# Kernel tuning notes

Measured on AMD Instinct MI355X. Metric: run time of the kernel, lower is better.

The kernel has to match this reference:

```python
import jax, jax.numpy as jnp
import numpy as np

B = 16384   # batch
D = 768     # in_features == out_features
H = 768     # expert_hidden_size (must equal D, see MoRALayer wiring)
E = 4       # num_experts_per_level
L = 2       # num_levels
K = 2       # SparseMoE top-k
T = 10      # max_act_steps
LN_EPS = 1e-5


def setup_inputs() -> dict:
    key = jax.random.key(0)
    ks = jax.random.split(key, 8)
    s = 0.02
    return {
        "x": jax.random.normal(ks[0], (B, D), jnp.float32),
        # LSTMCell params (torch gate order i,f,g,o)
        "Wi": jax.random.normal(ks[1], (4 * H, D), jnp.float32) * s,
        "Wh": jax.random.normal(ks[2], (4 * H, H), jnp.float32) * s,
        "bi": jnp.zeros((4 * H,), jnp.float32),
        "bh": jnp.zeros((4 * H,), jnp.float32),
        # halting head
        "Whalt": jax.random.normal(ks[3], (1, H), jnp.float32) * s,
        "bhalt": jnp.zeros((1,), jnp.float32),
        # hierarchical MoE params, stacked over levels (all dims equal: D==H)
        "gateW": jax.random.normal(ks[4], (L, E, H), jnp.float32) * s,
        "gateb": jnp.zeros((L, E), jnp.float32),
        "W1": jax.random.normal(ks[5], (L, E, H, H), jnp.float32) * s,
        "b1": jnp.zeros((L, E, H), jnp.float32),
        "W2": jax.random.normal(ks[6], (L, E, D, H), jnp.float32) * s,
        "b2": jnp.zeros((L, E, D), jnp.float32),
        # LayerNorm
        "gamma": jnp.ones((D,), jnp.float32),
        "beta": jnp.zeros((D,), jnp.float32),
    }


def _act(x, Wi, Wh, bi, bh, Whalt, bhalt):
    """AdaptiveComputationTime: fixed T LSTM steps (faithful worst-case of the
    data-dependent early break). Returns rem * mean_t(h_t) per the torch math:
    avg = sum_t(h_t * rem_final) / n_updates, with rem_final broadcast over t."""
    b = x.shape[0]
    h0 = jnp.zeros((b, H), x.dtype)
    c0 = jnp.zeros((b, H), x.dtype)
    hp0 = jnp.zeros((b, 1), x.dtype)
    rem0 = jnp.zeros((b, 1), x.dtype)
    hsum0 = jnp.zeros((b, H), x.dtype)
    xWi = x @ Wi.T + bi + bh  # constant across steps

    def step(carry, _):
        h, c, hp, rem, hsum = carry
        gates = xWi + h @ Wh.T
        i, f, g, o = jnp.split(gates, 4, axis=-1)
        c = jax.nn.sigmoid(f) * c + jax.nn.sigmoid(i) * jnp.tanh(g)
        h = jax.nn.sigmoid(o) * jnp.tanh(c)
        y = jax.nn.sigmoid(h @ Whalt.T + bhalt)  # [b,1]
        hp = hp + y * (1.0 - hp)
        rem = rem + 1.0 - hp
        return (h, c, hp, rem, hsum + h), None

    (h, c, hp, rem, hsum), _ = jax.lax.scan(
        step, (h0, c0, hp0, rem0, hsum0), None, length=T)
    n_updates = jnp.asarray(float(T), x.dtype)
    avg = rem * hsum / n_updates  # [b,H]
    return avg, hp, n_updates


def _sparse_moe(x, Wg, bg, W1, b1, W2, b2):
    """Top-k expert routing (intended semantics of the torch SparseMoE)."""
    logits = x @ Wg.T + bg                                   # [b,E]
    w, idx = jax.lax.top_k(logits, K)                        # [b,K]
    w = jax.nn.softmax(w, axis=-1)
    hmid = jax.nn.relu(jnp.einsum('bi,ehi->beh', x, W1) + b1)  # [b,E,H]
    eo = jnp.einsum('beh,eoh->beo', hmid, W2) + b2             # [b,E,D]
    sel = jnp.take_along_axis(eo, idx[:, :, None], axis=1)     # [b,K,D]
    return jnp.sum(w[:, :, None] * sel, axis=1)                # [b,D]


def reference(x, Wi, Wh, bi, bh, Whalt, bhalt,
              gateW, gateb, W1, b1, W2, b2, gamma, beta):
    h, _hp, _n = _act(x, Wi, Wh, bi, bh, Whalt, bhalt)
    for l in range(L):
        h = _sparse_moe(h, gateW[l], gateb[l], W1[l], b1[l], W2[l], b2[l])
    mu = jnp.mean(h, axis=-1, keepdims=True)
    var = jnp.mean(jnp.square(h - mu), axis=-1, keepdims=True)
    return (h - mu) * jax.lax.rsqrt(var + LN_EPS) * gamma + beta
```

## Files before the change

### kernel.cpp

```cpp
#include <hip/hip_runtime.h>
#include <cstdint>
#include <cstddef>

#define Bn 16384
#define Dn 768
#define Hn 768
#define G4 3072
#define Tn 10
#define LO_SCALE 4096.0f
#define LO_INV   (1.0f/4096.0f)

typedef _Float16 f16;
typedef _Float16 f16x8 __attribute__((ext_vector_type(8)));
typedef float    f32x4 __attribute__((ext_vector_type(4)));

__device__ __forceinline__ float fexp2(float x) { return __builtin_amdgcn_exp2f(x); }
__device__ __forceinline__ float frcp(float x)  { return __builtin_amdgcn_rcpf(x); }
__device__ __forceinline__ float fsigm(float x) { return frcp(1.f + fexp2(-1.44269504f * x)); }
__device__ __forceinline__ float ftanh(float x) { return 1.f - 2.f * frcp(1.f + fexp2(2.88539008f * x)); }

__device__ __forceinline__ void gll16(const void* g, void* l) {
    __builtin_amdgcn_global_load_lds((const __attribute__((address_space(1))) void*)g,
                                     (__attribute__((address_space(3))) void*)l, 16, 0, 0);
}

template <bool SPLIT, int EPI, bool BIAS, bool RELU>
__global__ __launch_bounds__(256) void mgemm(
    const f16* __restrict__ Ah, const f16* __restrict__ Al, int lda,
    const f16* __restrict__ Bh, const f16* __restrict__ Bl,
    float* __restrict__ Cf, f16* __restrict__ Ch, f16* __restrict__ Cl, int ldc,
    const float* __restrict__ bias,
    const float* __restrict__ xwi, float* __restrict__ cst, float* __restrict__ hsum,
    f16* __restrict__ hh_out, f16* __restrict__ hl_out,
    float* __restrict__ dhalt, const float* __restrict__ Whalt,
    long aZ, long bZ, long cZ, long biasZ)
{
    const int z = blockIdx.z;
    if (z) {
        Ah += (long)z * aZ; if (SPLIT) Al += (long)z * aZ;
        Bh += (long)z * bZ; if (SPLIT) Bl += (long)z * bZ;
        if (EPI == 0) Cf += (long)z * cZ;
        if (EPI == 1 || EPI == 2) { Ch += (long)z * cZ; if (EPI == 1) Cl += (long)z * cZ; }
        if (BIAS) bias += (long)z * biasZ;
    }
    constexpr int HALF = SPLIT ? 2 : 1;
    __shared__ __align__(16) f16 sA[2][HALF * 4096];
    __shared__ __align__(16) f16 sB[2][HALF * 4096];

    const int tid  = threadIdx.x;
    const int w    = tid >> 6, lane = tid & 63;
    const int quad = lane >> 4, l15 = lane & 15;
    const int n0 = blockIdx.x * 128, m0 = blockIdx.y * 128;
    const int wm = (w >> 1) * 64,   wn = (w & 1) * 64;

    const int sr0 = tid >> 2;
    const int sc0 = (((tid & 3) - (sr0 >> 1)) & 3);
    const int sr1 = (tid + 256) >> 2;
    const int sc1 = (((tid & 3) - (sr1 >> 1)) & 3);

    auto stage = [&](int sel, int k0) {
        gll16(Ah + (long)(m0 + sr0) * lda + k0 + sc0 * 8, &sA[sel][tid * 8]);
        gll16(Bh + (long)(n0 + sr0) * 768 + k0 + sc0 * 8, &sB[sel][tid * 8]);
        gll16(Ah + (long)(m0 + sr1) * lda + k0 + sc1 * 8, &sA[sel][(tid + 256) * 8]);
        gll16(Bh + (long)(n0 + sr1) * 768 + k0 + sc1 * 8, &sB[sel][(tid + 256) * 8]);
        if (SPLIT) {
            gll16(Al + (long)(m0 + sr0) * lda + k0 + sc0 * 8, &sA[sel][4096 + tid * 8]);
            gll16(Bl + (long)(n0 + sr0) * 768 + k0 + sc0 * 8, &sB[sel][4096 + tid * 8]);
            gll16(Al + (long)(m0 + sr1) * lda + k0 + sc1 * 8, &sA[sel][4096 + (tid + 256) * 8]);
            gll16(Bl + (long)(n0 + sr1) * 768 + k0 + sc1 * 8, &sB[sel][4096 + (tid + 256) * 8]);
        }
    };

    f32x4 acc[4][4], accx[4][4];
#pragma unroll
    for (int i = 0; i < 4; i++)
#pragma unroll
        for (int j = 0; j < 4; j++) {
            acc[i][j] = (f32x4){0.f, 0.f, 0.f, 0.f};
            if (SPLIT) accx[i][j] = (f32x4){0.f, 0.f, 0.f, 0.f};
        }

    stage(0, 0);
    for (int it = 0; it < 24; it++) {
        __syncthreads();
        if (it + 1 < 24) stage((it + 1) & 1, (it + 1) * 32);
        const int sel = it & 1;

        f16x8 ah[4], al[4], bh[4], bl[4];
#pragma unroll
        for (int t = 0; t < 4; t++) {
            int ra = wm + t * 16 + l15;
            int ca = (quad + (ra >> 1)) & 3;
            ah[t] = *(const f16x8*)&sA[sel][ra * 32 + ca * 8];
            if (SPLIT) al[t] = *(const f16x8*)&sA[sel][4096 + ra * 32 + ca * 8];
            int rb = wn + t * 16 + l15;
            int cb = (quad + (rb >> 1)) & 3;
            bh[t] = *(const f16x8*)&sB[sel][rb * 32 + cb * 8];
            if (SPLIT) bl[t] = *(const f16x8*)&sB[sel][4096 + rb * 32 + cb * 8];
        }
#pragma unroll
        for (int i = 0; i < 4; i++)
#pragma unroll
            for (int j = 0; j < 4; j++) {
                acc[i][j] = __builtin_amdgcn_mfma_f32_16x16x32_f16(ah[i], bh[j], acc[i][j], 0, 0, 0);
                if (SPLIT) {
                    accx[i][j] = __builtin_amdgcn_mfma_f32_16x16x32_f16(ah[i], bl[j], accx[i][j], 0, 0, 0);
                    accx[i][j] = __builtin_amdgcn_mfma_f32_16x16x32_f16(al[i], bh[j], accx[i][j], 0, 0, 0);
                }
            }
    }

    if (EPI == 3) {
        const int j = ((n0 + wn) >> 2) + l15;
        const float wj = Whalt[j];
#pragma unroll
        for (int i = 0; i < 4; i++) {
#pragma unroll
            for (int reg = 0; reg < 4; reg++) {
                int r = m0 + wm + i * 16 + quad * 4 + reg;
                long xb = (long)r * G4 + n0 + wn + l15;
                float iv = acc[i][0][reg] + accx[i][0][reg] * LO_INV + xwi[xb];
                float fv = acc[i][1][reg] + accx[i][1][reg] * LO_INV + xwi[xb + 16];
                float gv = acc[i][2][reg] + accx[i][2][reg] * LO_INV + xwi[xb + 32];
                float ov = acc[i][3][reg] + accx[i][3][reg] * LO_INV + xwi[xb + 48];
                long ci = (long)r * Hn + j;
                float cv = fsigm(fv) * cst[ci] + fsigm(iv) * ftanh(gv);
                float hv = fsigm(ov) * ftanh(cv);
                cst[ci] = cv;
                hsum[ci] += hv;
                f16 hh = (f16)hv;
                hh_out[ci] = hh;
                hl_out[ci] = (f16)((hv - (float)hh) * LO_SCALE);
                float p = hv * wj;
                p += __shfl_xor(p, 1, 16);
                p += __shfl_xor(p, 2, 16);
                p += __shfl_xor(p, 4, 16);
                p += __shfl_xor(p, 8, 16);
                if (l15 == 0) atomicAdd(&dhalt[r], p);
            }
        }
    } else {
#pragma unroll
        for (int i = 0; i < 4; i++)
#pragma unroll
            for (int j = 0; j < 4; j++) {
                int col = n0 + wn + j * 16 + l15;
                float bv = BIAS ? bias[col] : 0.f;
#pragma unroll
                for (int reg = 0; reg < 4; reg++) {
                    int r = m0 + wm + i * 16 + quad * 4 + reg;
                    float v = acc[i][j][reg] + (SPLIT ? accx[i][j][reg] * LO_INV : 0.f) + bv;
                    if (RELU) v = v > 0.f ? v : 0.f;
                    long o = (long)r * ldc + col;
                    if (EPI == 0) Cf[o] = v;
                    else if (EPI == 2) Ch[o] = (f16)v;
                    else {
                        f16 hh = (f16)v;
                        Ch[o] = hh;
                        Cl[o] = (f16)((v - (float)hh) * LO_SCALE);
                    }
                }
            }
    }
}


__global__ void split_plain_k(const float* __restrict__ src, f16* __restrict__ dh,
                              f16* __restrict__ dl, long n) {
    long i = (long)blockIdx.x * 256 + threadIdx.x;
    if (i < n) {
        float v = src[i];
        f16 h = (f16)v;
        dh[i] = h;
        dl[i] = (f16)((v - (float)h) * LO_SCALE);
    }
}

__global__ void split_perm_k(const float* __restrict__ src, f16* __restrict__ dh,
                             f16* __restrict__ dl) {
    int P = blockIdx.x;
    int q = ((P >> 4) & 3) * Hn + (P >> 6) * 16 + (P & 15);
    const float* s = src + (long)q * 768;
    long o = (long)P * 768;
#pragma unroll
    for (int u = 0; u < 3; u++) {
        int kk = threadIdx.x + u * 256;
        float v = s[kk];
        f16 h = (f16)v;
        dh[o + kk] = h;
        dl[o + kk] = (f16)((v - (float)h) * LO_SCALE);
    }
}

__global__ void bsum_perm_k(const float* __restrict__ bi, const float* __restrict__ bh,
                            float* __restrict__ bsum) {
    int P = blockIdx.x * 256 + threadIdx.x;
    if (P < G4) {
        int q = ((P >> 4) & 3) * Hn + (P >> 6) * 16 + (P & 15);
        bsum[P] = bi[q] + bh[q];
    }
}

__global__ __launch_bounds__(256) void lstm0_k(
    const float* __restrict__ xwi, float* __restrict__ cst, float* __restrict__ hsum,
    f16* __restrict__ hh, f16* __restrict__ hl, float* __restrict__ d0,
    const float* __restrict__ Whalt)
{
    const int row = blockIdx.x, tid = threadIdx.x;
    const float* xr = xwi + (long)row * G4;
    const long hb = (long)row * Hn;
    float part = 0.f;
#pragma unroll
    for (int u = 0; u < 3; u++) {
        int j = tid + u * 256;
        int Pb = (j >> 4) * 64 + (j & 15);
        float iv = xr[Pb], gv = xr[Pb + 32], ov = xr[Pb + 48];
        float cv = fsigm(iv) * ftanh(gv);
        float hv = fsigm(ov) * ftanh(cv);
        cst[hb + j] = cv;
        hsum[hb + j] = hv;
        f16 h = (f16)hv;
        hh[hb + j] = h;
        hl[hb + j] = (f16)((hv - (float)h) * LO_SCALE);
        part += hv * Whalt[j];
    }
    __shared__ float red[256];
    red[tid] = part;
    __syncthreads();
    for (int s = 128; s > 0; s >>= 1) {
        if (tid < s) red[tid] += red[tid + s];
        __syncthreads();
    }
    if (tid == 0) d0[row] = red[0];
}

__global__ void rem_k(const float* __restrict__ d, const float* __restrict__ bhalt,
                      float* __restrict__ rem, int bc) {
    int r = blockIdx.x * 256 + threadIdx.x;
    if (r >= bc) return;
    float b0 = bhalt[0];
    float prod = 1.f, rm = 0.f;
#pragma unroll
    for (int t = 0; t < Tn; t++) {
        float y = fsigm(d[(long)t * bc + r] + b0);
        prod *= (1.f - y);
        rm += prod;
    }
    rem[r] = rm;
}

__global__ void avgsplit_k(const float* __restrict__ hsum, const float* __restrict__ rem,
                           f16* __restrict__ xmh, f16* __restrict__ xml) {
    long i = (long)blockIdx.x * 256 + threadIdx.x;
    int row = (int)(i / Hn);
    float v = rem[row] * hsum[i] * (1.f / (float)Tn);
    f16 h = (f16)v;
    xmh[i] = h;
    xml[i] = (f16)((v - (float)h) * LO_SCALE);
}

__global__ __launch_bounds__(256) void moe_gate_k(
    const f16* __restrict__ xmh, const f16* __restrict__ xml,
    const float* __restrict__ gW, const float* __restrict__ gb,
    float* __restrict__ wout, int* __restrict__ idxout)
{
    const int row = blockIdx.x, tid = threadIdx.x;
    const long xb = (long)row * Hn;
    float p[4] = {0.f, 0.f, 0.f, 0.f};
#pragma unroll
    for (int u = 0; u < 3; u++) {
        int j = tid + u * 256;
        float xv = (float)xmh[xb + j] + (float)xml[xb + j] * LO_INV;
        p[0] += xv * gW[j];
        p[1] += xv * gW[Hn + j];
        p[2] += xv * gW[2 * Hn + j];
        p[3] += xv * gW[3 * Hn + j];
    }
    __shared__ float red[256];
    __shared__ float logit[4];
    for (int e = 0; e < 4; e++) {
        red[tid] = p[e];
        __syncthreads();
        for (int s = 128; s > 0; s >>= 1) {
            if (tid < s) red[tid] += red[tid + s];
            __syncthreads();
        }
        if (tid == 0) logit[e] = red[0] + gb[e];
        __syncthreads();
    }
    if (tid == 0) {
        int i0 = 0;
        for (int e = 1; e < 4; e++) if (logit[e] > logit[i0]) i0 = e;
        int i1 = -1;
        for (int e = 0; e < 4; e++) {
            if (e == i0) continue;
            if (i1 < 0 || logit[e] > logit[i1]) i1 = e;
        }
        float ex = expf(logit[i1] - logit[i0]);
        wout[2 * row] = 1.f / (1.f + ex);
        wout[2 * row + 1] = ex / (1.f + ex);
        idxout[2 * row] = i0;
        idxout[2 * row + 1] = i1;
    }
}

template <bool SO>
__global__ void combine_k(const float* __restrict__ eo, const float* __restrict__ wv,
                          const int* __restrict__ idx, float* __restrict__ dst,
                          f16* __restrict__ dh, f16* __restrict__ dl) {
    long i = (long)blockIdx.x * 256 + threadIdx.x;
    int row = (int)(i / Hn);
    int d = (int)(i - (long)row * Hn);
    long base = (long)row * G4;
    float v = wv[2 * row]     * eo[base + (long)idx[2 * row]     * Hn + d]
            + wv[2 * row + 1] * eo[base + (long)idx[2 * row + 1] * Hn + d];
    if (SO) {
        f16 h = (f16)v;
        dh[i] = h;
        dl[i] = (f16)((v - (float)h) * LO_SCALE);
    } else {
        dst[i] = v;
    }
}

__global__ __launch_bounds__(256) void layernorm_k(
    const float* __restrict__ in, const float* __restrict__ gamma,
    const float* __restrict__ beta, float* __restrict__ out)
{
    const int row = blockIdx.x, tid = threadIdx.x;
    const float* xr = in + (long)row * Dn;
    float v[3], s = 0.f, s2 = 0.f;
#pragma unroll
    for (int u = 0; u < 3; u++) {
        v[u] = xr[tid + u * 256];
        s += v[u];
        s2 += v[u] * v[u];
    }
    __shared__ float r1[256], r2[256];
    __shared__ float smu, srs;
    r1[tid] = s; r2[tid] = s2;
    __syncthreads();
    for (int st = 128; st > 0; st >>= 1) {
        if (tid < st) { r1[tid] += r1[tid + st]; r2[tid] += r2[tid + st]; }
        __syncthreads();
    }
    if (tid == 0) {
        float mu = r1[0] * (1.f / (float)Dn);
        float var = r2[0] * (1.f / (float)Dn) - mu * mu;
        smu = mu;
        srs = 1.f / sqrtf(var + 1e-5f);
    }
    __syncthreads();
    float mu = smu, rs = srs;
#pragma unroll
    for (int u = 0; u < 3; u++) {
        int j = tid + u * 256;
        out[(long)row * Dn + j] = (v[u] - mu) * rs * gamma[j] + beta[j];
    }
}


extern "C" void kernel_launch(void* const* d_in, const int* in_sizes, int n_in,
                              void* d_out, int out_size, void* d_ws, size_t ws_size,
                              hipStream_t stream) {
    (void)in_sizes; (void)n_in; (void)out_size;
    const float* x     = (const float*)d_in[0];
    const float* Wi    = (const float*)d_in[1];
    const float* Wh    = (const float*)d_in[2];
    const float* bi    = (const float*)d_in[3];
    const float* bh    = (const float*)d_in[4];
    const float* Whalt = (const float*)d_in[5];
    const float* bhalt = (const float*)d_in[6];
    const float* gateW = (const float*)d_in[7];
    const float* gateb = (const float*)d_in[8];
    const float* W1    = (const float*)d_in[9];
    const float* b1    = (const float*)d_in[10];
    const float* W2    = (const float*)d_in[11];
    const float* b2    = (const float*)d_in[12];
    const float* gamma = (const float*)d_in[13];
    const float* beta  = (const float*)d_in[14];
    float* out = (float*)d_out;

    char* p = (char*)d_ws;
    auto carve = [&](size_t bytes) { char* r = p; p += (bytes + 255) & ~(size_t)255; return r; };

    const long WIHN = (long)G4 * 768;
    const long WEHN = (long)8 * 768 * 768;
    f16* Wih = (f16*)carve(WIHN * 2); f16* Wil = (f16*)carve(WIHN * 2);
    f16* Whh = (f16*)carve(WIHN * 2); f16* Whl = (f16*)carve(WIHN * 2);
    f16* W1h = (f16*)carve(WEHN * 2); f16* W1l = (f16*)carve(WEHN * 2);
    f16* W2h = (f16*)carve(WEHN * 2); f16* W2l = (f16*)carve(WEHN * 2);
    float* bsum = (float*)carve(G4 * 4);
    size_t fixed = (size_t)(p - (char*)d_ws);

    int Bc = Bn;
    while (Bc > 128) {
        size_t need = fixed + (size_t)Bc * 34100 + 64 * 256;
        if (need <= ws_size) break;
        Bc >>= 1;
    }
    const int nChunks = Bn / Bc;

    float* xwi   = (float*)carve((size_t)Bc * G4 * 4);
    float* cst   = (float*)carve((size_t)Bc * 768 * 4);
    float* hsumb = (float*)carve((size_t)Bc * 768 * 4);
    char*  pool  = carve((size_t)Bc * 15360);
    float* d     = (float*)carve((size_t)Bc * Tn * 4);
    float* rem   = (float*)carve((size_t)Bc * 4);
    float* wbuf  = (float*)carve((size_t)Bc * 2 * 4);
    int*   ibuf  = (int*)carve((size_t)Bc * 2 * 4);

    f16* xh  = (f16*)pool;
    f16* xl  = xh + (size_t)Bc * 768;
    f16* h0h = xl + (size_t)Bc * 768;
    f16* h0l = h0h + (size_t)Bc * 768;
    f16* h1h = h0l + (size_t)Bc * 768;
    f16* h1l = h1h + (size_t)Bc * 768;
    f16* xmh = (f16*)pool;
    f16* xml = xmh + (size_t)Bc * 768;
    f16* hmh = xml + (size_t)Bc * 768;
    f16* hml = hmh + (size_t)Bc * G4;

    split_perm_k<<<G4, 256, 0, stream>>>(Wi, Wih, Wil);
    split_perm_k<<<G4, 256, 0, stream>>>(Wh, Whh, Whl);
    split_plain_k<<<(int)((WEHN + 255) / 256), 256, 0, stream>>>(W1, W1h, W1l, WEHN);
    split_plain_k<<<(int)((WEHN + 255) / 256), 256, 0, stream>>>(W2, W2h, W2l, WEHN);
    bsum_perm_k<<<G4 / 256, 256, 0, stream>>>(bi, bh, bsum);

    dim3 blk(256);
    dim3 g24(24, Bc / 128, 1);
    dim3 g6z(6, Bc / 128, 4);
    const int ew = Bc * 3;
    const long EXP_OFF = (long)4 * 768 * 768;

    for (int ch = 0; ch < nChunks; ch++) {
        const float* xc = x + (size_t)ch * Bc * Dn;
        float* outc = out + (size_t)ch * Bc * Dn;

        split_plain_k<<<ew, blk, 0, stream>>>(xc, xh, xl, (long)Bc * 768);

        mgemm<true, 0, true, false><<<g24, blk, 0, stream>>>(
            xh, xl, 768, Wih, Wil, xwi, nullptr, nullptr, G4, bsum,
            nullptr, nullptr, nullptr, nullptr, nullptr, nullptr, nullptr, 0, 0, 0, 0);

        hipMemsetAsync(d, 0, (size_t)Bc * Tn * 4, stream);
        lstm0_k<<<Bc, blk, 0, stream>>>(xwi, cst, hsumb, h0h, h0l, d, Whalt);

        for (int t = 1; t < Tn; t++) {
            f16* rah = (t & 1) ? h0h : h1h;
            f16* ral = (t & 1) ? h0l : h1l;
            f16* wah = (t & 1) ? h1h : h0h;
            f16* wal = (t & 1) ? h1l : h0l;
            mgemm<true, 3, false, false><<<g24, blk, 0, stream>>>(
                rah, ral, 768, Whh, Whl, nullptr, nullptr, nullptr, 0, nullptr,
                xwi, cst, hsumb, wah, wal, d + (size_t)t * Bc, Whalt, 0, 0, 0, 0);
        }

        rem_k<<<(Bc + 255) / 256, blk, 0, stream>>>(d, bhalt, rem, Bc);
        avgsplit_k<<<ew, blk, 0, stream>>>(hsumb, rem, xmh, xml);

        float* eo = xwi;
        for (int l = 0; l < 2; l++) {
            moe_gate_k<<<Bc, blk, 0, stream>>>(xmh, xml, gateW + (long)l * G4,
                                               gateb + l * 4, wbuf, ibuf);
            if (l == 0) {
                mgemm<true, 1, true, true><<<g24, blk, 0, stream>>>(
                    xmh, xml, 768, W1h, W1l, nullptr, hmh, hml, G4, b1,
                    nullptr, nullptr, nullptr, nullptr, nullptr, nullptr, nullptr, 0, 0, 0, 0);
                mgemm<true, 0, true, false><<<g6z, blk, 0, stream>>>(
                    hmh, hml, G4, W2h, W2l, eo, nullptr, nullptr, G4, b2,
                    nullptr, nullptr, nullptr, nullptr, nullptr, nullptr, nullptr,
                    768, (long)768 * 768, 768, 768);
                combine_k<true><<<ew, blk, 0, stream>>>(eo, wbuf, ibuf, nullptr, xmh, xml);
            } else {
                mgemm<false, 2, true, true><<<g24, blk, 0, stream>>>(
                    xmh, nullptr, 768, W1h + EXP_OFF, nullptr, nullptr, hmh, nullptr, G4,
                    b1 + G4, nullptr, nullptr, nullptr, nullptr, nullptr, nullptr, nullptr,
                    0, 0, 0, 0);
                mgemm<false, 0, true, false><<<g6z, blk, 0, stream>>>(
                    hmh, nullptr, G4, W2h + EXP_OFF, nullptr, eo, nullptr, nullptr, G4,
                    b2 + G4, nullptr, nullptr, nullptr, nullptr, nullptr, nullptr, nullptr,
                    768, (long)768 * 768, 768, 768);
                combine_k<false><<<ew, blk, 0, stream>>>(eo, wbuf, ibuf, hsumb, nullptr, nullptr);
            }
        }

        layernorm_k<<<Bc, blk, 0, stream>>>(hsumb, gamma, beta, outc);
    }
}
```

Before: 6.522 ms.

## Load B operand directly from global into registers, bypassing LDS

The B tile (weights) is no longer staged through shared memory. Each lane now reads its MFMA B fragments straight from global memory into registers, double-buffered across a manually unrolled two-stage K loop, while A is still staged through LDS. This halves the LDS footprint and removes the LDS write/read traffic for B, which could raise occupancy. In exchange it adds per-wave redundant global loads of B (both M-waves fetch the same columns) and more register pressure from the double-buffered fragments.

```diff
diff --git a/kernel.cpp b/kernel.cpp
--- a/kernel.cpp
+++ b/kernel.cpp
@@ -45,7 +45,6 @@
     }
     constexpr int HALF = SPLIT ? 2 : 1;
     __shared__ __align__(16) f16 sA[2][HALF * 4096];
-    __shared__ __align__(16) f16 sB[2][HALF * 4096];
 
     const int tid  = threadIdx.x;
     const int w    = tid >> 6, lane = tid & 63;
@@ -60,14 +59,21 @@
 
     auto stage = [&](int sel, int k0) {
         gll16(Ah + (long)(m0 + sr0) * lda + k0 + sc0 * 8, &sA[sel][tid * 8]);
-        gll16(Bh + (long)(n0 + sr0) * 768 + k0 + sc0 * 8, &sB[sel][tid * 8]);
         gll16(Ah + (long)(m0 + sr1) * lda + k0 + sc1 * 8, &sA[sel][(tid + 256) * 8]);
-        gll16(Bh + (long)(n0 + sr1) * 768 + k0 + sc1 * 8, &sB[sel][(tid + 256) * 8]);
         if (SPLIT) {
             gll16(Al + (long)(m0 + sr0) * lda + k0 + sc0 * 8, &sA[sel][4096 + tid * 8]);
-            gll16(Bl + (long)(n0 + sr0) * 768 + k0 + sc0 * 8, &sB[sel][4096 + tid * 8]);
             gll16(Al + (long)(m0 + sr1) * lda + k0 + sc1 * 8, &sA[sel][4096 + (tid + 256) * 8]);
-            gll16(Bl + (long)(n0 + sr1) * 768 + k0 + sc1 * 8, &sB[sel][4096 + (tid + 256) * 8]);
+        }
+    };
+
+    const f16* Bbase  = Bh + (long)(n0 + wn + l15) * 768 + quad * 8;
+    const f16* Bbasel = SPLIT ? (Bl + (long)(n0 + wn + l15) * 768 + quad * 8) : nullptr;
+
+    auto loadB = [&](int k0, f16x8* bh, f16x8* bl) {
+#pragma unroll
+        for (int t = 0; t < 4; t++) {
+            bh[t] = *(const f16x8*)(Bbase + (long)t * 12288 + k0);
+            if (SPLIT) bl[t] = *(const f16x8*)(Bbasel + (long)t * 12288 + k0);
         }
     };
 
@@ -80,23 +86,14 @@
             if (SPLIT) accx[i][j] = (f32x4){0.f, 0.f, 0.f, 0.f};
         }
 
-    stage(0, 0);
-    for (int it = 0; it < 24; it++) {
-        __syncthreads();
-        if (it + 1 < 24) stage((it + 1) & 1, (it + 1) * 32);
-        const int sel = it & 1;
-
-        f16x8 ah[4], al[4], bh[4], bl[4];
+    auto compute = [&](int sel, const f16x8* bh, const f16x8* bl) {
+        f16x8 ah[4], al[4];
 #pragma unroll
         for (int t = 0; t < 4; t++) {
             int ra = wm + t * 16 + l15;
             int ca = (quad + (ra >> 1)) & 3;
             ah[t] = *(const f16x8*)&sA[sel][ra * 32 + ca * 8];
             if (SPLIT) al[t] = *(const f16x8*)&sA[sel][4096 + ra * 32 + ca * 8];
-            int rb = wn + t * 16 + l15;
-            int cb = (quad + (rb >> 1)) & 3;
-            bh[t] = *(const f16x8*)&sB[sel][rb * 32 + cb * 8];
-            if (SPLIT) bl[t] = *(const f16x8*)&sB[sel][4096 + rb * 32 + cb * 8];
         }
 #pragma unroll
         for (int i = 0; i < 4; i++)
@@ -108,6 +105,22 @@
                     accx[i][j] = __builtin_amdgcn_mfma_f32_16x16x32_f16(al[i], bh[j], accx[i][j], 0, 0, 0);
                 }
             }
+    };
+
+    f16x8 b0h[4], b0l[4], b1h[4], b1l[4];
+    stage(0, 0);
+    loadB(0, b0h, b0l);
+    for (int ip = 0; ip < 12; ip++) {
+        __syncthreads();
+        stage(1, (2 * ip + 1) * 32);
+        loadB((2 * ip + 1) * 32, b1h, b1l);
+        compute(0, b0h, b0l);
+        __syncthreads();
+        if (ip < 11) {
+            stage(0, (2 * ip + 2) * 32);
+            loadB((2 * ip + 2) * 32, b0h, b0l);
+        }
+        compute(1, b1h, b1l);
     }
 
     if (EPI == 3) {
```

Result: slower. 7.486 ms (+14.8%).
